# Kernel tuning notes

Measured on AMD Instinct MI355X. Metric: run time of the kernel, lower is better.

## Reference

```python
import jax, jax.numpy as jnp
import numpy as np

B, N, D_IN, H, F = 2, 2048, 512, 8, 64
NEG_SLOPE = 0.2


def setup_inputs() -> dict:
    key = jax.random.key(0)
    k0, k1, k2, k3 = jax.random.split(key, 4)
    nodes = jax.random.normal(k0, (B, N, D_IN), dtype=jnp.float32)
    edges = jax.random.randint(k1, (B, N, N, 1), 0, 2).astype(jnp.int32)
    # ensure every node has at least one neighbor (self-loop) so softmax is finite
    idx = jnp.arange(N)
    edges = edges.at[:, idx, idx, :].set(1)
    W = jax.random.normal(k2, (D_IN, H * F), dtype=jnp.float32) * 0.02
    a = jax.random.normal(k3, (2 * F,), dtype=jnp.float32) * 0.02
    return {"nodes": nodes, "edges": edges, "W": W, "a": a}


def reference(nodes, edges, W, a):
    b, n, _ = nodes.shape
    mapped = (nodes @ W).reshape(b, n, H, F)  # [B,N,H,F]
    # additive attention: attn([m_i ; m_j]) = a_l . m_i + a_r . m_j
    a_l, a_r = a[:F], a[F:]
    el = jnp.einsum('bnhf,f->bnh', mapped, a_l)
    er = jnp.einsum('bnhf,f->bnh', mapped, a_r)
    scores = jax.nn.leaky_relu(el[:, :, None, :] + er[:, None, :, :], negative_slope=NEG_SLOPE)  # [B,N,N,H]
    mask = edges != 0  # [B,N,N,1] broadcasts over heads
    scores = jnp.where(mask, scores, -jnp.inf)
    attn_weights = jax.nn.softmax(scores, axis=2)  # softmax over neighbors j
    attn_res = jnp.einsum('bijh,bjhf->bihf', attn_weights, mapped)  # [B,N,H,F]
    # is_concat=False path: mean over heads, then sigmoid
    return jax.nn.sigmoid(attn_res.mean(axis=2))  # [B,N,F]
```

## Files before the change

### kernel.cpp

```cpp
#include <hip/hip_runtime.h>
#include <hip/hip_bf16.h>
#include <math.h>

#define Bq   2
#define Nq   2048
#define DIN  512
#define Hq   8
#define Fq   64
#define NEG  0.2f

using short8 = __attribute__((ext_vector_type(8))) short;
using f32x4  = __attribute__((ext_vector_type(4))) float;

__device__ inline unsigned int bf16_rne(float x) {
    unsigned int u = __float_as_uint(x);
    u += 0x7fffu + ((u >> 16) & 1u);
    return u >> 16;
}

#define AFRAG_BLOCKS 256
#define WFRAG_BLOCKS 128

__global__ __launch_bounds__(256) void prep_kernel(
    const float* __restrict__ nodes, ushort* __restrict__ Afrag,
    const float* __restrict__ W,     ushort* __restrict__ Wfrag)
{
    __shared__ __align__(16) char smem[16 * 516 * 4];
    const int bid = blockIdx.x;
    const int t   = threadIdx.x;

    if (bid < AFRAG_BLOCKS) {
        float (*As)[516] = (float(*)[516])smem;
        const int mt = bid;
        {
            const int row = t >> 4, c = t & 15;
#pragma unroll
            for (int i = 0; i < 8; i++) {
                float4 v = *(const float4*)&nodes[((size_t)mt * 16 + row) * DIN + (c + i * 16) * 4];
                *(float4*)&As[row][(c + i * 16) * 4] = v;
            }
        }
        __syncthreads();
        const int lane = t & 63, ksg = t >> 6;
        const int quad = lane >> 4, l15 = lane & 15;
#pragma unroll
        for (int k2 = 0; k2 < 4; k2++) {
            int ks = ksg * 4 + k2;
            const float* src = &As[l15][ks * 32 + quad * 8];
            float4 f0 = *(const float4*)src;
            float4 f1 = *(const float4*)(src + 4);
            uint4 pk;
            pk.x = bf16_rne(f0.x) | (bf16_rne(f0.y) << 16);
            pk.y = bf16_rne(f0.z) | (bf16_rne(f0.w) << 16);
            pk.z = bf16_rne(f1.x) | (bf16_rne(f1.y) << 16);
            pk.w = bf16_rne(f1.z) | (bf16_rne(f1.w) << 16);
            *(uint4*)(Afrag + ((size_t)(mt * 16 + ks) * 64 + lane) * 8) = pk;
        }
        return;
    }

    {
        float (*Ws)[68] = (float(*)[68])smem;
        const int id = bid - AFRAG_BLOCKS;
        const int ks = id & 15, h = id >> 4;
        {
            const int row = t >> 3, c = t & 7;
            const float* src = &W[(size_t)(ks * 32 + row) * (Hq * Fq) + h * 64 + c * 8];
            float4 v0 = *(const float4*)src;
            float4 v1 = *(const float4*)(src + 4);
            *(float4*)&Ws[row][c * 8]     = v0;
            *(float4*)&Ws[row][c * 8 + 4] = v1;
        }
        __syncthreads();
        const int lane = t & 63, nf = t >> 6;
        const int quad = lane >> 4, l15 = lane & 15;
        float f[8];
#pragma unroll
        for (int jj = 0; jj < 8; jj++) f[jj] = Ws[quad * 8 + jj][nf * 16 + l15];
        uint4 pk;
        pk.x = bf16_rne(f[0]) | (bf16_rne(f[1]) << 16);
        pk.y = bf16_rne(f[2]) | (bf16_rne(f[3]) << 16);
        pk.z = bf16_rne(f[4]) | (bf16_rne(f[5]) << 16);
        pk.w = bf16_rne(f[6]) | (bf16_rne(f[7]) << 16);
        *(uint4*)(Wfrag + (((size_t)(h * 16 + ks) * 4 + nf) * 64 + lane) * 8) = pk;
    }
}

#define GEMM_BLOCKS 512
#define PACK_BLOCKS 1024

__global__ __launch_bounds__(256) void work_kernel(
    const ushort* __restrict__ Afrag, const ushort* __restrict__ Wfrag,
    const float*  __restrict__ avec,
    ushort* __restrict__ Vfrag,
    float* __restrict__ el_t,
    float* __restrict__ er_t,
    float* __restrict__ E_t,
    float* __restrict__ F_t,
    const int* __restrict__ edges, unsigned int* __restrict__ ebT)
{
    const int bid = blockIdx.x;
    const int t   = threadIdx.x;

    if (bid >= GEMM_BLOCKS) {
        int gid = (bid - GEMM_BLOCKS) * 256 + t;
        int i = gid & 2047;
        int w = (gid >> 11) & 63;
        int b = gid >> 17;
        const int4* ep = (const int4*)(edges + (((size_t)b * Nq + i) * Nq + w * 32));
        unsigned int word = 0;
#pragma unroll
        for (int c = 0; c < 8; c++) {
            int4 v = ep[c];
            word |= (v.x != 0 ? 1u : 0u) << (c * 4);
            word |= (v.y != 0 ? 1u : 0u) << (c * 4 + 1);
            word |= (v.z != 0 ? 1u : 0u) << (c * 4 + 2);
            word |= (v.w != 0 ? 1u : 0u) << (c * 4 + 3);
        }
        ebT[((size_t)b * 64 + w) * Nq + i] = word;
        return;
    }

    const int lane = t & 63;
    const int wv   = t >> 6;
    const int quad = lane >> 4;
    const int l15  = lane & 15;
    const int h    = bid >> 6;
    const int mt   = (bid & 63) * 4 + wv;
    const int row0 = mt * 16;

    const ushort* ap = Afrag + (size_t)mt * 8192 + lane * 8;
    const ushort* bp = Wfrag + (size_t)h * 32768 + lane * 8;

    f32x4 zero4 = {0.f, 0.f, 0.f, 0.f};
    f32x4 acc[4] = {zero4, zero4, zero4, zero4};

    short8 a0, a1, b0[4], b1[4];
    a0 = *(const short8*)(ap);
#pragma unroll
    for (int nf = 0; nf < 4; nf++) b0[nf] = *(const short8*)(bp + nf * 512);

    for (int ks = 0; ks < 16; ks += 2) {
        a1 = *(const short8*)(ap + (ks + 1) * 512);
#pragma unroll
        for (int nf = 0; nf < 4; nf++) b1[nf] = *(const short8*)(bp + (ks + 1) * 2048 + nf * 512);
#pragma unroll
        for (int nf = 0; nf < 4; nf++)
            acc[nf] = __builtin_amdgcn_mfma_f32_16x16x32_bf16(a0, b0[nf], acc[nf], 0, 0, 0);
        a0 = *(const short8*)(ap + (ks + 2) * 512);
#pragma unroll
        for (int nf = 0; nf < 4; nf++) b0[nf] = *(const short8*)(bp + (ks + 2) * 2048 + nf * 512);
#pragma unroll
        for (int nf = 0; nf < 4; nf++)
            acc[nf] = __builtin_amdgcn_mfma_f32_16x16x32_bf16(a1, b1[nf], acc[nf], 0, 0, 0);
    }

    float aL[4], aR[4];
#pragma unroll
    for (int nf = 0; nf < 4; nf++) {
        aL[nf] = avec[nf * 16 + l15];
        aR[nf] = avec[Fq + nf * 16 + l15];
    }
    const int bb = row0 >> 11;
    const int bh = bb * Hq + h;
#pragma unroll
    for (int r = 0; r < 4; r++) {
        float pl = acc[0][r] * aL[0] + acc[1][r] * aL[1] + acc[2][r] * aL[2] + acc[3][r] * aL[3];
        float pr = acc[0][r] * aR[0] + acc[1][r] * aR[1] + acc[2][r] * aR[2] + acc[3][r] * aR[3];
#pragma unroll
        for (int off = 1; off < 16; off <<= 1) {
            pl += __shfl_xor(pl, off, 64);
            pr += __shfl_xor(pr, off, 64);
        }
        if (l15 == 0) {
            int n = (row0 + quad * 4 + r) & (Nq - 1);
            el_t[(size_t)bh * Nq + n] = pl;
            er_t[(size_t)bh * Nq + n] = pr;
            E_t[(size_t)bh * Nq + n]  = __expf(pr);
            F_t[(size_t)bh * Nq + n]  = __expf(NEG * pr);
        }
    }

    const int n_base = row0 & (Nq - 1);
    const int sblk   = n_base >> 5;
    const int quadp  = ((wv & 1) << 1) | (quad >> 1);
    const int jj0    = (quad & 1) * 4;
#pragma unroll
    for (int nf = 0; nf < 4; nf++) {
        unsigned int r0 = bf16_rne(acc[nf][0]), r1 = bf16_rne(acc[nf][1]);
        unsigned int r2 = bf16_rne(acc[nf][2]), r3 = bf16_rne(acc[nf][3]);
        uint2 pk;
        pk.x = r0 | (r1 << 16);
        pk.y = r2 | (r3 << 16);
        size_t off = ((((size_t)bh * 64 + sblk) * 4 + nf) * 64 + quadp * 16 + l15) * 8 + jj0;
        *(uint2*)(Vfrag + off) = pk;
    }
}

__global__ __launch_bounds__(256, 2) void attn_kernel(
    const float* __restrict__ el_t, const float* __restrict__ er_t,
    const float* __restrict__ E_t,  const float* __restrict__ F_t,
    const ushort* __restrict__ Vfrag,
    const unsigned int* __restrict__ ebT, float* __restrict__ attn)
{
    const int lane = threadIdx.x & 63;
    const int kh   = threadIdx.x >> 6;
    const int quad = lane >> 4;
    const int l15  = lane & 15;
    const int bid  = blockIdx.x;
    const int it   = bid & 31;
    const int h    = (bid >> 5) & 7;
    const int b    = bid >> 8;
    const int bh   = b * Hq + h;
    const int i0   = it * 64;

    __shared__ float smax[4];
    __shared__ float lds_l[4][4][16];
    __shared__ __align__(16) float lds_acc[4][4][4][64][4];

    const float* errow = er_t + (size_t)bh * Nq;
    float mx = -INFINITY;
#pragma unroll
    for (int ii = 0; ii < 8; ii++) mx = fmaxf(mx, errow[threadIdx.x + ii * 256]);
#pragma unroll
    for (int off = 32; off > 0; off >>= 1) mx = fmaxf(mx, __shfl_xor(mx, off, 64));
    if (lane == 0) smax[kh] = mx;
    __syncthreads();
    const float emax = fmaxf(fmaxf(smax[0], smax[1]), fmaxf(smax[2], smax[3]));

    float Acf[4], Ccf[4], Tcf[4];
#pragma unroll
    for (int rs = 0; rs < 4; rs++) {
        float elv = el_t[(size_t)bh * Nq + i0 + rs * 16 + l15];
        float xm  = elv + emax;
        float m   = fmaxf(xm, NEG * xm);
        Acf[rs] = __expf(elv - m);
        Ccf[rs] = __expf(NEG * elv - m);
        Tcf[rs] = __expf(-elv);
    }

    const float*        Ep  = E_t + (size_t)bh * Nq + kh * 512;
    const float*        Fp  = F_t + (size_t)bh * Nq + kh * 512;
    const ushort*       vp  = Vfrag + (size_t)bh * 131072 + kh * 32768 + lane * 8;
    const unsigned int* e0p = ebT + ((size_t)b * 64 + kh * 16) * Nq + i0 + l15;

    f32x4 zero4 = {0.f, 0.f, 0.f, 0.f};
    f32x4 acc[4][4];
#pragma unroll
    for (int rs = 0; rs < 4; rs++)
#pragma unroll
        for (int nf = 0; nf < 4; nf++) acc[rs][nf] = zero4;
    float lsum[4] = {0.f, 0.f, 0.f, 0.f};

    for (int s = 0; s < 16; s++) {
        short8 vb0 = *(const short8*)(vp + s * 2048);
        short8 vb1 = *(const short8*)(vp + s * 2048 + 512);
        short8 vb2 = *(const short8*)(vp + s * 2048 + 1024);
        short8 vb3 = *(const short8*)(vp + s * 2048 + 1536);
        unsigned int w[4];
#pragma unroll
        for (int rs = 0; rs < 4; rs++) w[rs] = e0p[(size_t)s * Nq + rs * 16];
        float4 Ea = *(const float4*)(Ep + s * 32 + quad * 8);
        float4 Eb = *(const float4*)(Ep + s * 32 + quad * 8 + 4);
        float4 Fa = *(const float4*)(Fp + s * 32 + quad * 8);
        float4 Fb = *(const float4*)(Fp + s * 32 + quad * 8 + 4);
        float E8[8] = {Ea.x, Ea.y, Ea.z, Ea.w, Eb.x, Eb.y, Eb.z, Eb.w};
        float F8[8] = {Fa.x, Fa.y, Fa.z, Fa.w, Fb.x, Fb.y, Fb.z, Fb.w};

#pragma unroll
        for (int rs = 0; rs < 4; rs++) {
            const unsigned int wq = w[rs] >> (quad * 8);
            union { short8 s8; unsigned int w4[4]; } af;
#pragma unroll
            for (int pp = 0; pp < 4; pp++) {
                unsigned int ua = 0, ub = 0;
#pragma unroll
                for (int q2 = 0; q2 < 2; q2++) {
                    const int jj = pp * 2 + q2;
                    float e  = E8[jj];
                    float fv = F8[jj];
                    bool sel = e > Tcf[rs];
                    float p  = (sel ? Acf[rs] : Ccf[rs]) * (sel ? e : fv);
                    int  k   = ((int)(wq << (31 - jj))) >> 31;
                    unsigned int u = __float_as_uint(p) & (unsigned int)k;
                    lsum[rs] += __uint_as_float(u);
                    if (q2 == 0) ua = u; else ub = u;
                }
                af.w4[pp] = __builtin_amdgcn_perm(ub, ua, 0x07060302);
            }
            acc[rs][0] = __builtin_amdgcn_mfma_f32_16x16x32_bf16(af.s8, vb0, acc[rs][0], 0, 0, 0);
            acc[rs][1] = __builtin_amdgcn_mfma_f32_16x16x32_bf16(af.s8, vb1, acc[rs][1], 0, 0, 0);
            acc[rs][2] = __builtin_amdgcn_mfma_f32_16x16x32_bf16(af.s8, vb2, acc[rs][2], 0, 0, 0);
            acc[rs][3] = __builtin_amdgcn_mfma_f32_16x16x32_bf16(af.s8, vb3, acc[rs][3], 0, 0, 0);
        }
    }

#pragma unroll
    for (int rs = 0; rs < 4; rs++) {
        lsum[rs] += __shfl_xor(lsum[rs], 16, 64);
        lsum[rs] += __shfl_xor(lsum[rs], 32, 64);
    }
    if (quad == 0) {
#pragma unroll
        for (int rs = 0; rs < 4; rs++) lds_l[kh][rs][l15] = lsum[rs];
    }

#pragma unroll
    for (int rs = 0; rs < 4; rs++)
#pragma unroll
        for (int nf = 0; nf < 4; nf++)
            *(f32x4*)&lds_acc[kh][rs][nf][lane][0] = acc[rs][nf];
    __syncthreads();

    const int rs = kh;
    f32x4 facc[4] = {zero4, zero4, zero4, zero4};
#pragma unroll
    for (int k2 = 0; k2 < 4; k2++)
#pragma unroll
        for (int nf = 0; nf < 4; nf++) {
            f32x4 v = *(const f32x4*)&lds_acc[k2][rs][nf][lane][0];
            facc[nf][0] += v[0]; facc[nf][1] += v[1];
            facc[nf][2] += v[2]; facc[nf][3] += v[3];
        }
    float flr[4];
#pragma unroll
    for (int r = 0; r < 4; r++) {
        float sl = 0.f;
#pragma unroll
        for (int k2 = 0; k2 < 4; k2++) sl += lds_l[k2][rs][quad * 4 + r];
        flr[r] = sl;
    }
#pragma unroll
    for (int nf = 0; nf < 4; nf++)
#pragma unroll
        for (int r = 0; r < 4; r++)
            attn[(((size_t)b * Nq + i0 + rs * 16 + quad * 4 + r) * Hq + h) * Fq + nf * 16 + l15]
                = facc[nf][r] / flr[r];
}

__global__ __launch_bounds__(256) void out_kernel(
    const float* __restrict__ attn, float* __restrict__ out)
{
    const int idx = blockIdx.x * 256 + threadIdx.x;
    const int f   = idx & 63;
    const int bn  = idx >> 6;
    const float* p = attn + (size_t)bn * Hq * Fq + f;
    float s = 0.f;
#pragma unroll
    for (int h = 0; h < Hq; h++) s += p[h * Fq];
    s *= (1.f / Hq);
    out[idx] = 1.f / (1.f + __expf(-s));
}

extern "C" void kernel_launch(void* const* d_in, const int* in_sizes, int n_in,
                              void* d_out, int out_size, void* d_ws, size_t ws_size,
                              hipStream_t stream) {
    const float* nodes = (const float*)d_in[0];
    const int*   edges = (const int*)d_in[1];
    const float* W     = (const float*)d_in[2];
    const float* a     = (const float*)d_in[3];
    float* out = (float*)d_out;

    char* ws = (char*)d_ws;
    ushort* Afrag = (ushort*)ws;           ws += (size_t)Bq * Nq * DIN * 2;
    ushort* Wfrag = (ushort*)ws;           ws += (size_t)DIN * Hq * Fq * 2;
    ushort* Vfrag = (ushort*)ws;           ws += (size_t)Bq * Hq * Nq * Fq * 2;
    float*  el_t  = (float*)ws;            ws += (size_t)Bq * Hq * Nq * 4;
    float*  er_t  = (float*)ws;            ws += (size_t)Bq * Hq * Nq * 4;
    float*  E_t   = (float*)ws;            ws += (size_t)Bq * Hq * Nq * 4;
    float*  F_t   = (float*)ws;            ws += (size_t)Bq * Hq * Nq * 4;
    unsigned int* ebT = (unsigned int*)ws; ws += (size_t)Bq * (Nq / 32) * Nq * 4;
    float*  attn  = (float*)ws;

    prep_kernel<<<AFRAG_BLOCKS + WFRAG_BLOCKS, 256, 0, stream>>>(nodes, Afrag, W, Wfrag);
    work_kernel<<<GEMM_BLOCKS + PACK_BLOCKS, 256, 0, stream>>>(
        Afrag, Wfrag, a, Vfrag, el_t, er_t, E_t, F_t, edges, ebT);
    attn_kernel<<<Bq * Hq * (Nq / 64), 256, 0, stream>>>(el_t, er_t, E_t, F_t, Vfrag, ebT, attn);
    out_kernel<<<(Bq * Nq * Fq) / 256, 256, 0, stream>>>(attn, out);
}
```

Baseline: 122.1 us.

## Switch attention inner loop to packed fp16 math with byte-mask edges and MFMA row sums

The attention probability computation moves from scalar fp32 with per-element select to packed half2 multiplies. Leaky-relu is applied as a max of the two exp branches. The edge mask is stored as byte masks (0xFF per neighbor) and applied with perm/AND instead of bit extraction, and the softmax denominator is accumulated with an extra MFMA against a ones vector instead of scalar adds. V and the E/F exponentials are stored in fp16, which cuts inner-loop ALU work but makes the mask buffer 8x larger and adds fp16 range/precision risk for the exponentials.

```diff
diff --git a/kernel.cpp b/kernel.cpp
--- a/kernel.cpp
+++ b/kernel.cpp
@@ -10,12 +10,19 @@
 #define NEG  0.2f
 
 using short8 = __attribute__((ext_vector_type(8))) short;
+using half8  = __attribute__((ext_vector_type(8))) _Float16;
+using half2v = __attribute__((ext_vector_type(2))) _Float16;
 using f32x4  = __attribute__((ext_vector_type(4))) float;
 
 __device__ inline unsigned int bf16_rne(float x) {
     unsigned int u = __float_as_uint(x);
     u += 0x7fffu + ((u >> 16) & 1u);
     return u >> 16;
+}
+__device__ inline unsigned int f16u(float x) {
+    union { _Float16 h; unsigned short u; } cv;
+    cv.h = (_Float16)x;
+    return (unsigned int)cv.u;
 }
 
 #define AFRAG_BLOCKS 256
@@ -87,7 +94,7 @@
 }
 
 #define GEMM_BLOCKS 512
-#define PACK_BLOCKS 1024
+#define PACK_BLOCKS 4096
 
 __global__ __launch_bounds__(256) void work_kernel(
     const ushort* __restrict__ Afrag, const ushort* __restrict__ Wfrag,
@@ -95,29 +102,27 @@
     ushort* __restrict__ Vfrag,
     float* __restrict__ el_t,
     float* __restrict__ er_t,
-    float* __restrict__ E_t,
-    float* __restrict__ F_t,
-    const int* __restrict__ edges, unsigned int* __restrict__ ebT)
+    unsigned int* __restrict__ EF_t,
+    const int* __restrict__ edges, uint2* __restrict__ ebTB)
 {
     const int bid = blockIdx.x;
     const int t   = threadIdx.x;
 
     if (bid >= GEMM_BLOCKS) {
         int gid = (bid - GEMM_BLOCKS) * 256 + t;
-        int i = gid & 2047;
-        int w = (gid >> 11) & 63;
-        int b = gid >> 17;
-        const int4* ep = (const int4*)(edges + (((size_t)b * Nq + i) * Nq + w * 32));
-        unsigned int word = 0;
-#pragma unroll
-        for (int c = 0; c < 8; c++) {
-            int4 v = ep[c];
-            word |= (v.x != 0 ? 1u : 0u) << (c * 4);
-            word |= (v.y != 0 ? 1u : 0u) << (c * 4 + 1);
-            word |= (v.z != 0 ? 1u : 0u) << (c * 4 + 2);
-            word |= (v.w != 0 ? 1u : 0u) << (c * 4 + 3);
-        }
-        ebT[((size_t)b * 64 + w) * Nq + i] = word;
+        int i  = gid & 2047;
+        int jb = (gid >> 11) & 255;
+        int b  = gid >> 19;
+        const int4* ep = (const int4*)(edges + (((size_t)b * Nq + i) * Nq + jb * 8));
+        int4 v0 = ep[0];
+        int4 v1 = ep[1];
+        unsigned int lo = 0, hi = 0;
+        lo |= v0.x ? 0x000000FFu : 0u;  lo |= v0.y ? 0x0000FF00u : 0u;
+        lo |= v0.z ? 0x00FF0000u : 0u;  lo |= v0.w ? 0xFF000000u : 0u;
+        hi |= v1.x ? 0x000000FFu : 0u;  hi |= v1.y ? 0x0000FF00u : 0u;
+        hi |= v1.z ? 0x00FF0000u : 0u;  hi |= v1.w ? 0xFF000000u : 0u;
+        uint2 w; w.x = lo; w.y = hi;
+        ebTB[((size_t)(b * 256 + jb)) * 2048 + i] = w;
         return;
     }
 
@@ -176,8 +181,8 @@
             int n = (row0 + quad * 4 + r) & (Nq - 1);
             el_t[(size_t)bh * Nq + n] = pl;
             er_t[(size_t)bh * Nq + n] = pr;
-            E_t[(size_t)bh * Nq + n]  = __expf(pr);
-            F_t[(size_t)bh * Nq + n]  = __expf(NEG * pr);
+            float E = __expf(pr), F = __expf(NEG * pr);
+            EF_t[(size_t)bh * Nq + n] = f16u(E) | (f16u(F) << 16);
         }
     }
 
@@ -187,11 +192,9 @@
     const int jj0    = (quad & 1) * 4;
 #pragma unroll
     for (int nf = 0; nf < 4; nf++) {
-        unsigned int r0 = bf16_rne(acc[nf][0]), r1 = bf16_rne(acc[nf][1]);
-        unsigned int r2 = bf16_rne(acc[nf][2]), r3 = bf16_rne(acc[nf][3]);
         uint2 pk;
-        pk.x = r0 | (r1 << 16);
-        pk.y = r2 | (r3 << 16);
+        pk.x = f16u(acc[nf][0]) | (f16u(acc[nf][1]) << 16);
+        pk.y = f16u(acc[nf][2]) | (f16u(acc[nf][3]) << 16);
         size_t off = ((((size_t)bh * 64 + sblk) * 4 + nf) * 64 + quadp * 16 + l15) * 8 + jj0;
         *(uint2*)(Vfrag + off) = pk;
     }
@@ -199,9 +202,9 @@
 
 __global__ __launch_bounds__(256, 2) void attn_kernel(
     const float* __restrict__ el_t, const float* __restrict__ er_t,
-    const float* __restrict__ E_t,  const float* __restrict__ F_t,
+    const unsigned int* __restrict__ EF_t,
     const ushort* __restrict__ Vfrag,
-    const unsigned int* __restrict__ ebT, float* __restrict__ attn)
+    const uint2* __restrict__ ebTB, float* __restrict__ attn)
 {
     const int lane = threadIdx.x & 63;
     const int kh   = threadIdx.x >> 6;
@@ -228,81 +231,71 @@
     __syncthreads();
     const float emax = fmaxf(fmaxf(smax[0], smax[1]), fmaxf(smax[2], smax[3]));
 
-    float Acf[4], Ccf[4], Tcf[4];
+    union HU { unsigned int u; half2v h; };
+    HU AC2[4];
 #pragma unroll
     for (int rs = 0; rs < 4; rs++) {
         float elv = el_t[(size_t)bh * Nq + i0 + rs * 16 + l15];
         float xm  = elv + emax;
         float m   = fmaxf(xm, NEG * xm);
-        Acf[rs] = __expf(elv - m);
-        Ccf[rs] = __expf(NEG * elv - m);
-        Tcf[rs] = __expf(-elv);
-    }
-
-    const float*        Ep  = E_t + (size_t)bh * Nq + kh * 512;
-    const float*        Fp  = F_t + (size_t)bh * Nq + kh * 512;
+        float A = __expf(elv - m);
+        float C = __expf(NEG * elv - m);
+        AC2[rs].u = f16u(A) | (f16u(C) << 16);
+    }
+
+    const unsigned int* EFp = EF_t + (size_t)bh * Nq + kh * 512;
     const ushort*       vp  = Vfrag + (size_t)bh * 131072 + kh * 32768 + lane * 8;
-    const unsigned int* e0p = ebT + ((size_t)b * 64 + kh * 16) * Nq + i0 + l15;
+    const uint2*        mp  = ebTB + ((size_t)(b * 256 + kh * 64 + quad)) * 2048 + i0 + l15;
 
     f32x4 zero4 = {0.f, 0.f, 0.f, 0.f};
     f32x4 acc[4][4];
-#pragma unroll
-    for (int rs = 0; rs < 4; rs++)
+    f32x4 accl[4];
+#pragma unroll
+    for (int rs = 0; rs < 4; rs++) {
+        accl[rs] = zero4;
 #pragma unroll
         for (int nf = 0; nf < 4; nf++) acc[rs][nf] = zero4;
-    float lsum[4] = {0.f, 0.f, 0.f, 0.f};
+    }
+
+    const _Float16 one16 = (_Float16)1.0f;
+    const half8 onesv = {one16, one16, one16, one16, one16, one16, one16, one16};
 
     for (int s = 0; s < 16; s++) {
-        short8 vb0 = *(const short8*)(vp + s * 2048);
-        short8 vb1 = *(const short8*)(vp + s * 2048 + 512);
-        short8 vb2 = *(const short8*)(vp + s * 2048 + 1024);
-        short8 vb3 = *(const short8*)(vp + s * 2048 + 1536);
-        unsigned int w[4];
-#pragma unroll
-        for (int rs = 0; rs < 4; rs++) w[rs] = e0p[(size_t)s * Nq + rs * 16];
-        float4 Ea = *(const float4*)(Ep + s * 32 + quad * 8);
-        float4 Eb = *(const float4*)(Ep + s * 32 + quad * 8 + 4);
-        float4 Fa = *(const float4*)(Fp + s * 32 + quad * 8);
-        float4 Fb = *(const float4*)(Fp + s * 32 + quad * 8 + 4);
-        float E8[8] = {Ea.x, Ea.y, Ea.z, Ea.w, Eb.x, Eb.y, Eb.z, Eb.w};
-        float F8[8] = {Fa.x, Fa.y, Fa.z, Fa.w, Fb.x, Fb.y, Fb.z, Fb.w};
+        half8 vb0 = *(const half8*)(vp + s * 2048);
+        half8 vb1 = *(const half8*)(vp + s * 2048 + 512);
+        half8 vb2 = *(const half8*)(vp + s * 2048 + 1024);
+        half8 vb3 = *(const half8*)(vp + s * 2048 + 1536);
+        uint2 mbs[4];
+#pragma unroll
+        for (int rs = 0; rs < 4; rs++) mbs[rs] = mp[(size_t)s * 8192 + rs * 16];
+        uint4 efa = *(const uint4*)(EFp + s * 32 + quad * 8);
+        uint4 efb = *(const uint4*)(EFp + s * 32 + quad * 8 + 4);
+        unsigned int ef[8] = {efa.x, efa.y, efa.z, efa.w, efb.x, efb.y, efb.z, efb.w};
 
 #pragma unroll
         for (int rs = 0; rs < 4; rs++) {
-            const unsigned int wq = w[rs] >> (quad * 8);
-            union { short8 s8; unsigned int w4[4]; } af;
+            union AFU { half8 h8; unsigned int w4[4]; } af;
 #pragma unroll
             for (int pp = 0; pp < 4; pp++) {
-                unsigned int ua = 0, ub = 0;
-#pragma unroll
-                for (int q2 = 0; q2 < 2; q2++) {
-                    const int jj = pp * 2 + q2;
-                    float e  = E8[jj];
-                    float fv = F8[jj];
-                    bool sel = e > Tcf[rs];
-                    float p  = (sel ? Acf[rs] : Ccf[rs]) * (sel ? e : fv);
-                    int  k   = ((int)(wq << (31 - jj))) >> 31;
-                    unsigned int u = __float_as_uint(p) & (unsigned int)k;
-                    lsum[rs] += __uint_as_float(u);
-                    if (q2 == 0) ua = u; else ub = u;
-                }
-                af.w4[pp] = __builtin_amdgcn_perm(ub, ua, 0x07060302);
+                HU e0, e1, p0, p1, X, Y, P;
+                e0.u = ef[2 * pp];
+                e1.u = ef[2 * pp + 1];
+                p0.h = AC2[rs].h * e0.h;
+                p1.h = AC2[rs].h * e1.h;
+                X.u = __builtin_amdgcn_perm(p1.u, p0.u, 0x05040100);
+                Y.u = __builtin_amdgcn_perm(p1.u, p0.u, 0x07060302);
+                P.h = __builtin_elementwise_max(X.h, Y.h);
+                unsigned int msrc = (pp < 2) ? mbs[rs].x : mbs[rs].y;
+                unsigned int msel = (pp & 1) ? 0x03030202u : 0x01010000u;
+                unsigned int mw   = __builtin_amdgcn_perm(0u, msrc, msel);
+                af.w4[pp] = P.u & mw;
             }
-            acc[rs][0] = __builtin_amdgcn_mfma_f32_16x16x32_bf16(af.s8, vb0, acc[rs][0], 0, 0, 0);
-            acc[rs][1] = __builtin_amdgcn_mfma_f32_16x16x32_bf16(af.s8, vb1, acc[rs][1], 0, 0, 0);
-            acc[rs][2] = __builtin_amdgcn_mfma_f32_16x16x32_bf16(af.s8, vb2, acc[rs][2], 0, 0, 0);
-            acc[rs][3] = __builtin_amdgcn_mfma_f32_16x16x32_bf16(af.s8, vb3, acc[rs][3], 0, 0, 0);
-        }
-    }
-
-#pragma unroll
-    for (int rs = 0; rs < 4; rs++) {
-        lsum[rs] += __shfl_xor(lsum[rs], 16, 64);
-        lsum[rs] += __shfl_xor(lsum[rs], 32, 64);
-    }
-    if (quad == 0) {
-#pragma unroll
-        for (int rs = 0; rs < 4; rs++) lds_l[kh][rs][l15] = lsum[rs];
+            acc[rs][0] = __builtin_amdgcn_mfma_f32_16x16x32_f16(af.h8, vb0, acc[rs][0], 0, 0, 0);
+            acc[rs][1] = __builtin_amdgcn_mfma_f32_16x16x32_f16(af.h8, vb1, acc[rs][1], 0, 0, 0);
+            acc[rs][2] = __builtin_amdgcn_mfma_f32_16x16x32_f16(af.h8, vb2, acc[rs][2], 0, 0, 0);
+            acc[rs][3] = __builtin_amdgcn_mfma_f32_16x16x32_f16(af.h8, vb3, acc[rs][3], 0, 0, 0);
+            accl[rs]   = __builtin_amdgcn_mfma_f32_16x16x32_f16(af.h8, onesv, accl[rs], 0, 0, 0);
+        }
     }
 
 #pragma unroll
@@ -310,6 +303,13 @@
 #pragma unroll
         for (int nf = 0; nf < 4; nf++)
             *(f32x4*)&lds_acc[kh][rs][nf][lane][0] = acc[rs][nf];
+    if (l15 == 0) {
+#pragma unroll
+        for (int rs = 0; rs < 4; rs++)
+#pragma unroll
+            for (int r = 0; r < 4; r++)
+                lds_l[kh][rs][quad * 4 + r] = accl[rs][r];
+    }
     __syncthreads();
 
     const int rs = kh;
@@ -367,14 +367,13 @@
     ushort* Vfrag = (ushort*)ws;           ws += (size_t)Bq * Hq * Nq * Fq * 2;
     float*  el_t  = (float*)ws;            ws += (size_t)Bq * Hq * Nq * 4;
     float*  er_t  = (float*)ws;            ws += (size_t)Bq * Hq * Nq * 4;
-    float*  E_t   = (float*)ws;            ws += (size_t)Bq * Hq * Nq * 4;
-    float*  F_t   = (float*)ws;            ws += (size_t)Bq * Hq * Nq * 4;
-    unsigned int* ebT = (unsigned int*)ws; ws += (size_t)Bq * (Nq / 32) * Nq * 4;
+    unsigned int* EF_t = (unsigned int*)ws; ws += (size_t)Bq * Hq * Nq * 4;
+    uint2*  ebTB  = (uint2*)ws;            ws += (size_t)Bq * Nq * Nq;
     float*  attn  = (float*)ws;
 
     prep_kernel<<<AFRAG_BLOCKS + WFRAG_BLOCKS, 256, 0, stream>>>(nodes, Afrag, W, Wfrag);
     work_kernel<<<GEMM_BLOCKS + PACK_BLOCKS, 256, 0, stream>>>(
-        Afrag, Wfrag, a, Vfrag, el_t, er_t, E_t, F_t, edges, ebT);
-    attn_kernel<<<Bq * Hq * (Nq / 64), 256, 0, stream>>>(el_t, er_t, E_t, F_t, Vfrag, ebT, attn);
+        Afrag, Wfrag, a, Vfrag, el_t, er_t, EF_t, edges, ebTB);
+    attn_kernel<<<Bq * Hq * (Nq / 64), 256, 0, stream>>>(el_t, er_t, EF_t, Vfrag, ebTB, attn);
     out_kernel<<<(Bq * Nq * Fq) / 256, 256, 0, stream>>>(attn, out);
 }
```

Result: faster. 116.9 us (-4.2%).
